# Optimization experiments

Measured on AMD Instinct MI355X. Metric: run time of the kernel, lower is better.

The kernel has to match this reference:

```python
import jax, jax.numpy as jnp
import numpy as np

NUM_HEADS = 4
HEAD_DIM = 64
BN_EPS = 1e-5


def setup_inputs() -> dict:
    key = jax.random.key(0)
    ks = jax.random.split(key, 6)
    B, C, H, W = 8, 256, 48, 48
    HD = NUM_HEADS * HEAD_DIM  # 256
    x = jax.random.normal(ks[0], (B, C, H, W), dtype=jnp.float32)
    q_w = jax.random.normal(ks[1], (HD, C), dtype=jnp.float32) * (1.0 / np.sqrt(C))
    k_w = jax.random.normal(ks[2], (HEAD_DIM, C), dtype=jnp.float32) * (1.0 / np.sqrt(C))
    v_w = jax.random.normal(ks[3], (HEAD_DIM, C), dtype=jnp.float32) * (1.0 / np.sqrt(C))
    proj_w = jax.random.normal(ks[4], (C, HD), dtype=jnp.float32) * (1.0 / np.sqrt(HD))
    proj_b = jnp.zeros((C,), dtype=jnp.float32)
    gamma = jnp.ones((C,), dtype=jnp.float32)
    beta = jnp.zeros((C,), dtype=jnp.float32)
    return {"x": x, "q_w": q_w, "k_w": k_w, "v_w": v_w,
            "proj_w": proj_w, "proj_b": proj_b, "gamma": gamma, "beta": beta}


def reference(x, q_w, k_w, v_w, proj_w, proj_b, gamma, beta):
    B, C, H, W = x.shape
    N = H * W
    scale = HEAD_DIM ** -0.5
    xf = x.reshape(B, C, N)  # 1x1 conv == channel matmul
    q = jnp.einsum('oc,bcn->bon', q_w, xf).reshape(B, NUM_HEADS, HEAD_DIM, N)
    k = jnp.einsum('dc,bcn->bdn', k_w, xf)  # shared single KV head (MQA)
    v = jnp.einsum('dc,bcn->bdn', v_w, xf)
    # scores: [B, heads, N, N]
    attn = jnp.einsum('bhdn,bdm->bhnm', q, k) * scale
    attn = jax.nn.softmax(attn, axis=-1)
    out = jnp.einsum('bhnm,bdm->bhdn', attn, v)  # [B, heads, d, N]
    out = out.reshape(B, NUM_HEADS * HEAD_DIM, N)
    out = jnp.einsum('co,bon->bcn', proj_w, out) + proj_b[None, :, None]
    out = out.reshape(B, C, H, W)
    # BatchNorm2d (training-mode batch statistics, biased variance)
    mean = jnp.mean(out, axis=(0, 2, 3), keepdims=True)
    var = jnp.var(out, axis=(0, 2, 3), keepdims=True)
    out = gamma[None, :, None, None] * (out - mean) * jax.lax.rsqrt(var + BN_EPS) + beta[None, :, None, None]
    return out + x
```

## Files before the change

### kernel.cpp

```cpp
#include <hip/hip_runtime.h>
#include <hip/hip_bf16.h>
#include <math.h>

#define BB 8
#define CCH 256
#define NN 2304
#define NH 4
#define HDIM 64
#define QKV_ROWS 384
#define BN_EPS 1e-5f
#define NTILES 36
#define SLOG2E 0.18033688011112042f

typedef short bf16x8 __attribute__((ext_vector_type(8)));
typedef float f32x4 __attribute__((ext_vector_type(4)));

#if __has_builtin(__builtin_amdgcn_exp2f)
#define EXP2(x) __builtin_amdgcn_exp2f(x)
#else
#define EXP2(x) __expf((x) * 0.6931471805599453f)
#endif

__device__ __forceinline__ unsigned bfpair(float a, float b) {
    __hip_bfloat162 h = __float22bfloat162_rn(make_float2(a, b));
    return *(unsigned*)&h;
}
__device__ __forceinline__ unsigned short f2bf(float f) {
    unsigned u = __float_as_uint(f);
    u = (u + 0x7FFFu + ((u >> 16) & 1u)) >> 16;
    return (unsigned short)u;
}

__global__ __launch_bounds__(256) void cvt_x_k(
    const float* __restrict__ x, unsigned short* __restrict__ xT)
{
    __shared__ float sX[64][65];
    const int tid = threadIdx.x;
    const int b  = blockIdx.x;
    const int nb = blockIdx.y * 64;
    const int cb = blockIdx.z * 64;

    #pragma unroll
    for (int u = 0; u < 4; ++u) {
        int c  = (tid >> 4) + 16 * u;
        int n4 = (tid & 15) * 4;
        float4 v = *(const float4*)(x + ((size_t)(b * CCH + cb + c)) * NN + nb + n4);
        sX[c][n4+0] = v.x; sX[c][n4+1] = v.y; sX[c][n4+2] = v.z; sX[c][n4+3] = v.w;
    }
    __syncthreads();

    const int n  = tid >> 2;
    const int cg = (tid & 3) * 16;
    unsigned vals[8];
    #pragma unroll
    for (int p = 0; p < 8; ++p)
        vals[p] = bfpair(sX[cg + 2*p][n], sX[cg + 2*p + 1][n]);
    unsigned short* dst = xT + ((size_t)(b * NN + nb + n)) * CCH + cb + cg;
    *(uint4*)dst = make_uint4(vals[0], vals[1], vals[2], vals[3]);
    *(uint4*)(dst + 8) = make_uint4(vals[4], vals[5], vals[6], vals[7]);
}

__global__ __launch_bounds__(256) void cvt_w_k(
    const float* __restrict__ qw, const float* __restrict__ kw,
    const float* __restrict__ vw, const float* __restrict__ pw,
    unsigned short* __restrict__ Wb, unsigned short* __restrict__ Pb)
{
    int idx = blockIdx.x * 256 + threadIdx.x;
    if (idx < 98304) {
        int o = idx >> 8, c = idx & 255;
        float v;
        if (o < 256)      v = qw[(size_t)o * CCH + c] * SLOG2E;
        else if (o < 320) v = kw[(size_t)(o - 256) * CCH + c];
        else              v = vw[(size_t)(o - 320) * CCH + c];
        Wb[idx] = f2bf(v);
    } else {
        int j = idx - 98304;
        if (j < 65536) Pb[j] = f2bf(pw[j]);
    }
}

__global__ __launch_bounds__(128) void qkv_mfma_k(
    const unsigned short* __restrict__ Wb, const unsigned short* __restrict__ xT,
    unsigned short* __restrict__ Qt, unsigned short* __restrict__ Kt,
    unsigned short* __restrict__ Vn)
{
    __shared__ unsigned short sE[2][64 * 72];
    const int tid = threadIdx.x;
    const int wave = tid >> 6;
    const int lane = tid & 63;
    const int quad = lane >> 4;
    const int l15  = lane & 15;
    const int b  = blockIdx.x;
    const int nb = blockIdx.y * 64;
    const int mb = blockIdx.z * 128 + wave * 64;

    const unsigned short* Ab = Wb + (size_t)(mb + l15) * CCH + quad * 8;
    const unsigned short* Bb = xT + ((size_t)(b * NN + nb + l15)) * CCH + quad * 8;

    f32x4 C[4][4] = {};
    for (int k0 = 0; k0 < CCH; k0 += 32) {
        bf16x8 aA[4], bB[4];
        #pragma unroll
        for (int i = 0; i < 4; ++i) aA[i] = *(const bf16x8*)(Ab + (size_t)(16*i) * CCH + k0);
        #pragma unroll
        for (int j = 0; j < 4; ++j) bB[j] = *(const bf16x8*)(Bb + (size_t)(16*j) * CCH + k0);
        #pragma unroll
        for (int i = 0; i < 4; ++i)
            #pragma unroll
            for (int j = 0; j < 4; ++j)
                C[i][j] = __builtin_amdgcn_mfma_f32_16x16x32_bf16(aA[i], bB[j], C[i][j], 0, 0, 0);
    }

    unsigned short* sEw = &sE[wave][0];
    if (mb < 320) {
        #pragma unroll
        for (int i = 0; i < 4; ++i)
            #pragma unroll
            for (int j = 0; j < 4; ++j) {
                unsigned p01 = bfpair(C[i][j][0], C[i][j][1]);
                unsigned p23 = bfpair(C[i][j][2], C[i][j][3]);
                unsigned short* p = sEw + (16*j + l15) * 72 + 16*i + quad*4;
                *(unsigned*)p = p01;
                *(unsigned*)(p + 2) = p23;
            }
        if (mb < 256) {
            #pragma unroll
            for (int it = 0; it < 8; ++it) {
                int flat = lane + 64 * it;
                int row = flat >> 3;
                int o8  = (flat & 7) * 8;
                uint4 v = *(const uint4*)(sEw + row * 72 + o8);
                *(uint4*)(Qt + ((size_t)(b * NN + nb + row)) * CCH + mb + o8) = v;
            }
        } else {
            #pragma unroll
            for (int it = 0; it < 8; ++it) {
                int flat = lane + 64 * it;
                int row = flat >> 3;
                int o8  = (flat & 7) * 8;
                uint4 v = *(const uint4*)(sEw + row * 72 + o8);
                *(uint4*)(Kt + ((size_t)(b * NN + nb + row)) * 64 + o8) = v;
            }
        }
    } else {
        #pragma unroll
        for (int i = 0; i < 4; ++i)
            #pragma unroll
            for (int j = 0; j < 4; ++j) {
                unsigned p01 = bfpair(C[i][j][0], C[i][j][1]);
                unsigned p23 = bfpair(C[i][j][2], C[i][j][3]);
                unsigned short* p = sEw + (16*i + quad*4) * 72 + 16*j + l15;
                p[0]   = (unsigned short)p01;
                p[72]  = (unsigned short)(p01 >> 16);
                p[144] = (unsigned short)p23;
                p[216] = (unsigned short)(p23 >> 16);
            }
        #pragma unroll
        for (int it = 0; it < 8; ++it) {
            int flat = lane + 64 * it;
            int row = flat >> 3;
            int n8  = (flat & 7) * 8;
            uint4 v = *(const uint4*)(sEw + row * 72 + n8);
            *(uint4*)(Vn + ((size_t)(b * 64 + (mb - 320) + row)) * NN + nb + n8) = v;
        }
    }
}

__global__ __launch_bounds__(256) void attn_k(
    const unsigned short* __restrict__ Qt,
    const unsigned short* __restrict__ Kt,
    const unsigned short* __restrict__ Vn,
    unsigned short* __restrict__ Ao)
{
    __shared__ __align__(16) char smem[36864];
    unsigned short* sK = (unsigned short*)smem;
    unsigned short* sV = (unsigned short*)(smem + 9216);
    unsigned short* sP = (unsigned short*)(smem + 18432);
    unsigned short* sT = (unsigned short*)smem;

    const int tid  = threadIdx.x;
    const int wave = tid >> 6;
    const int lane = tid & 63;
    const int quad = lane >> 4;
    const int l15  = lane & 15;
    const int hloc = wave >> 1;
    const int qoff = (wave & 1) * 32;
    const int b    = blockIdx.x;
    const int nb   = blockIdx.y * 64;
    const int head = blockIdx.z * 2 + hloc;

    unsigned short* sPh = sP + hloc * 64 * 72;

    bf16x8 aQ[2][2];
    const unsigned short* QtB = Qt + ((size_t)(b * NN + nb + qoff + l15)) * CCH + head * 64 + quad * 8;
    #pragma unroll
    for (int i = 0; i < 2; ++i)
        #pragma unroll
        for (int s = 0; s < 2; ++s)
            aQ[i][s] = *(const bf16x8*)(QtB + (size_t)(16*i) * CCH + s * 32);

    const int srow = tid >> 3;
    const int sch  = (tid & 7) * 8;

    bf16x8 pK[2], pV[2];
    #pragma unroll
    for (int u = 0; u < 2; ++u) {
        int row = srow + 32 * u;
        pK[u] = *(const bf16x8*)(Kt + ((size_t)(b * NN + row)) * 64 + sch);
        pV[u] = *(const bf16x8*)(Vn + ((size_t)(b * 64 + row)) * NN + sch);
    }

    f32x4 O[2][4] = {};
    float lacc[2][4] = {};

    for (int t = 0; t < NTILES; ++t) {
        __syncthreads();
        #pragma unroll
        for (int u = 0; u < 2; ++u) {
            int row = srow + 32 * u;
            *(bf16x8*)(sK + row * 72 + sch) = pK[u];
            *(bf16x8*)(sV + row * 72 + sch) = pV[u];
        }
        __syncthreads();

        if (t + 1 < NTILES) {
            const int m0n = (t + 1) * 64;
            #pragma unroll
            for (int u = 0; u < 2; ++u) {
                int row = srow + 32 * u;
                pK[u] = *(const bf16x8*)(Kt + ((size_t)(b * NN + m0n + row)) * 64 + sch);
                pV[u] = *(const bf16x8*)(Vn + ((size_t)(b * 64 + row)) * NN + m0n + sch);
            }
        }

        f32x4 C[2][4] = {};
        #pragma unroll
        for (int s = 0; s < 2; ++s)
            #pragma unroll
            for (int j = 0; j < 4; ++j) {
                bf16x8 bK = *(const bf16x8*)(sK + (16*j + l15) * 72 + s * 32 + quad * 8);
                C[0][j] = __builtin_amdgcn_mfma_f32_16x16x32_bf16(aQ[0][s], bK, C[0][j], 0, 0, 0);
                C[1][j] = __builtin_amdgcn_mfma_f32_16x16x32_bf16(aQ[1][s], bK, C[1][j], 0, 0, 0);
            }

        #pragma unroll
        for (int i = 0; i < 2; ++i)
            #pragma unroll
            for (int j = 0; j < 4; ++j) {
                float p0 = EXP2(C[i][j][0]);
                float p1 = EXP2(C[i][j][1]);
                float p2 = EXP2(C[i][j][2]);
                float p3 = EXP2(C[i][j][3]);
                lacc[i][0] += p0; lacc[i][1] += p1; lacc[i][2] += p2; lacc[i][3] += p3;
                unsigned p01 = bfpair(p0, p1);
                unsigned p23 = bfpair(p2, p3);
                unsigned short* bp = sPh + (qoff + 16*i + quad*4) * 72 + 16*j + l15;
                bp[0]   = (unsigned short)p01;
                bp[72]  = (unsigned short)(p01 >> 16);
                bp[144] = (unsigned short)p23;
                bp[216] = (unsigned short)(p23 >> 16);
            }

        #pragma unroll
        for (int s = 0; s < 2; ++s) {
            bf16x8 aP0 = *(const bf16x8*)(sPh + (qoff +  0 + l15) * 72 + s * 32 + quad * 8);
            bf16x8 aP1 = *(const bf16x8*)(sPh + (qoff + 16 + l15) * 72 + s * 32 + quad * 8);
            #pragma unroll
            for (int jd = 0; jd < 4; ++jd) {
                bf16x8 bV = *(const bf16x8*)(sV + (16*jd + l15) * 72 + s * 32 + quad * 8);
                O[0][jd] = __builtin_amdgcn_mfma_f32_16x16x32_bf16(aP0, bV, O[0][jd], 0, 0, 0);
                O[1][jd] = __builtin_amdgcn_mfma_f32_16x16x32_bf16(aP1, bV, O[1][jd], 0, 0, 0);
            }
        }
    }

    float rinv[2][4];
    #pragma unroll
    for (int i = 0; i < 2; ++i)
        #pragma unroll
        for (int r = 0; r < 4; ++r) {
            float s = lacc[i][r];
            s += __shfl_xor(s, 1);
            s += __shfl_xor(s, 2);
            s += __shfl_xor(s, 4);
            s += __shfl_xor(s, 8);
            rinv[i][r] = 1.0f / s;
        }

    __syncthreads();
    #pragma unroll
    for (int i = 0; i < 2; ++i)
        #pragma unroll
        for (int jd = 0; jd < 4; ++jd)
            #pragma unroll
            for (int r = 0; r < 4; ++r)
                sT[(qoff + 16*i + quad*4 + r) * 136 + hloc * 64 + 16*jd + l15] =
                    f2bf(O[i][jd][r] * rinv[i][r]);
    __syncthreads();

    #pragma unroll
    for (int it = 0; it < 4; ++it) {
        int flat = tid + 256 * it;
        int row = flat >> 4;
        int c8  = (flat & 15) * 8;
        uint4 v = *(const uint4*)(sT + row * 136 + c8);
        *(uint4*)(Ao + ((size_t)(b * NN + nb + row)) * CCH + blockIdx.z * 128 + c8) = v;
    }
}

__global__ __launch_bounds__(128) void proj_mfma_k(
    const unsigned short* __restrict__ Pb, const unsigned short* __restrict__ Ao,
    const float* __restrict__ pb, float* __restrict__ proj)
{
    __shared__ float sF[2][64 * 68];
    const int tid = threadIdx.x;
    const int wave = tid >> 6;
    const int lane = tid & 63;
    const int quad = lane >> 4;
    const int l15  = lane & 15;
    const int b  = blockIdx.x;
    const int nb = blockIdx.y * 64;
    const int mb = blockIdx.z * 128 + wave * 64;

    const unsigned short* Ab = Pb + (size_t)(mb + l15) * CCH + quad * 8;
    const unsigned short* Bb = Ao + ((size_t)(b * NN + nb + l15)) * CCH + quad * 8;

    f32x4 C[4][4] = {};
    for (int k0 = 0; k0 < CCH; k0 += 32) {
        bf16x8 aA[4], bB[4];
        #pragma unroll
        for (int i = 0; i < 4; ++i) aA[i] = *(const bf16x8*)(Ab + (size_t)(16*i) * CCH + k0);
        #pragma unroll
        for (int j = 0; j < 4; ++j) bB[j] = *(const bf16x8*)(Bb + (size_t)(16*j) * CCH + k0);
        #pragma unroll
        for (int i = 0; i < 4; ++i)
            #pragma unroll
            for (int j = 0; j < 4; ++j)
                C[i][j] = __builtin_amdgcn_mfma_f32_16x16x32_bf16(aA[i], bB[j], C[i][j], 0, 0, 0);
    }

    float* sFw = &sF[wave][0];
    #pragma unroll
    for (int i = 0; i < 4; ++i)
        #pragma unroll
        for (int r = 0; r < 4; ++r) {
            float bias = pb[mb + 16*i + quad*4 + r];
            #pragma unroll
            for (int j = 0; j < 4; ++j)
                sFw[(16*i + quad*4 + r) * 68 + 16*j + l15] = C[i][j][r] + bias;
        }
    #pragma unroll
    for (int it = 0; it < 16; ++it) {
        int flat = lane + 64 * it;
        int row = flat >> 4;
        int ch  = (flat & 15) * 4;
        f32x4 v = *(const f32x4*)(sFw + row * 68 + ch);
        *(f32x4*)(proj + ((size_t)(b * CCH + mb + row)) * NN + nb + ch) = v;
    }
}

__global__ __launch_bounds__(256) void bn_stats_k(
    const float* __restrict__ proj, const float* __restrict__ gamma,
    const float* __restrict__ beta, float* __restrict__ stats)
{
    const int c = blockIdx.x;
    const int tid = threadIdx.x;
    float s = 0.f, s2 = 0.f;
    for (int b = 0; b < BB; ++b) {
        const float* p = proj + ((size_t)b * CCH + c) * NN;
        for (int n = tid * 4; n < NN; n += 1024) {
            float4 v = *(const float4*)(p + n);
            s  += v.x + v.y + v.z + v.w;
            s2 += v.x*v.x + v.y*v.y + v.z*v.z + v.w*v.w;
        }
    }
    __shared__ float rs[256], rs2[256];
    rs[tid] = s; rs2[tid] = s2;
    __syncthreads();
    for (int off = 128; off > 0; off >>= 1) {
        if (tid < off) { rs[tid] += rs[tid + off]; rs2[tid] += rs2[tid + off]; }
        __syncthreads();
    }
    if (tid == 0) {
        const float inv_n = 1.0f / (float)(BB * NN);
        float mean = rs[0] * inv_n;
        float var  = rs2[0] * inv_n - mean * mean;
        float sc = gamma[c] * rsqrtf(var + BN_EPS);
        stats[c] = sc;
        stats[CCH + c] = beta[c] - mean * sc;
    }
}

__global__ __launch_bounds__(256) void bn_apply_k(
    const float* __restrict__ proj, const float* __restrict__ x,
    const float* __restrict__ stats, float* __restrict__ out)
{
    size_t idx = ((size_t)blockIdx.x * 256 + threadIdx.x) * 4;
    const size_t total = (size_t)BB * CCH * NN;
    if (idx >= total) return;
    int c = (int)((idx / NN) % CCH);
    float sc = stats[c], sh = stats[CCH + c];
    float4 p  = *(const float4*)(proj + idx);
    float4 xv = *(const float4*)(x + idx);
    float4 r;
    r.x = sc * p.x + sh + xv.x;
    r.y = sc * p.y + sh + xv.y;
    r.z = sc * p.z + sh + xv.z;
    r.w = sc * p.w + sh + xv.w;
    *(float4*)(out + idx) = r;
}

extern "C" void kernel_launch(void* const* d_in, const int* in_sizes, int n_in,
                              void* d_out, int out_size, void* d_ws, size_t ws_size,
                              hipStream_t stream)
{
    const float* x     = (const float*)d_in[0];
    const float* qw    = (const float*)d_in[1];
    const float* kw    = (const float*)d_in[2];
    const float* vw    = (const float*)d_in[3];
    const float* pw    = (const float*)d_in[4];
    const float* pb    = (const float*)d_in[5];
    const float* gamma = (const float*)d_in[6];
    const float* beta  = (const float*)d_in[7];
    float* out = (float*)d_out;

    char* ws = (char*)d_ws;
    unsigned short* xT = (unsigned short*)ws;
    unsigned short* Ao = (unsigned short*)ws;
    unsigned short* Wb = (unsigned short*)(ws + 9437184);
    unsigned short* Pb = (unsigned short*)(ws + 9633792);
    unsigned short* Qt = (unsigned short*)(ws + 9764864);
    unsigned short* Kt = (unsigned short*)(ws + 19202048);
    unsigned short* Vn = (unsigned short*)(ws + 21561344);
    float* proj  = (float*)(ws + 9764864);
    float* stats = (float*)(ws + 28639232);

    cvt_w_k<<<640, 256, 0, stream>>>(qw, kw, vw, pw, Wb, Pb);

    dim3 g0(BB, NN / 64, CCH / 64);
    cvt_x_k<<<g0, 256, 0, stream>>>(x, xT);

    dim3 g1(BB, NN / 64, 3);
    qkv_mfma_k<<<g1, 128, 0, stream>>>(Wb, xT, Qt, Kt, Vn);

    dim3 g2(BB, NN / 64, NH / 2);
    attn_k<<<g2, 256, 0, stream>>>(Qt, Kt, Vn, Ao);

    dim3 g3(BB, NN / 64, 2);
    proj_mfma_k<<<g3, 128, 0, stream>>>(Pb, Ao, pb, proj);

    bn_stats_k<<<CCH, 256, 0, stream>>>(proj, gamma, beta, stats);

    int total4 = BB * CCH * NN / 4;
    bn_apply_k<<<(total4 + 255) / 256, 256, 0, stream>>>(proj, x, stats, out);
}
```

Baseline: 224.6 us.

## Keep attention probabilities in registers, fuse BN stats into projection, store bf16

The attention kernel is restructured to one head per 128-thread block. It computes transposed scores (K times Q) so the exponentiated probabilities feed the PV MFMA directly from registers as 16x16x16 operands, removing the LDS round trip for P. The projection kernel now adds bias, reduces per-channel sum and sum of squares via shuffles and atomics, and stores the output as bf16. This replaces the separate BN statistics pass and halves the intermediate traffic. The risks are extra rounding from bf16 storage and from single-pass variance, plus atomic contention.

```diff
diff --git a/kernel.cpp b/kernel.cpp
--- a/kernel.cpp
+++ b/kernel.cpp
@@ -13,6 +13,7 @@
 #define SLOG2E 0.18033688011112042f
 
 typedef short bf16x8 __attribute__((ext_vector_type(8)));
+typedef short bf16x4 __attribute__((ext_vector_type(4)));
 typedef float f32x4 __attribute__((ext_vector_type(4)));
 
 #if __has_builtin(__builtin_amdgcn_exp2f)
@@ -21,6 +22,9 @@
 #define EXP2(x) __expf((x) * 0.6931471805599453f)
 #endif
 
+#define MFMA16(a, b, c) __builtin_amdgcn_mfma_f32_16x16x16bf16_1k(a, b, c, 0, 0, 0)
+#define MFMA32(a, b, c) __builtin_amdgcn_mfma_f32_16x16x32_bf16(a, b, c, 0, 0, 0)
+
 __device__ __forceinline__ unsigned bfpair(float a, float b) {
     __hip_bfloat162 h = __float22bfloat162_rn(make_float2(a, b));
     return *(unsigned*)&h;
@@ -29,6 +33,15 @@
     unsigned u = __float_as_uint(f);
     u = (u + 0x7FFFu + ((u >> 16) & 1u)) >> 16;
     return (unsigned short)u;
+}
+__device__ __forceinline__ bf16x4 pack4(float p0, float p1, float p2, float p3) {
+    union { unsigned u[2]; bf16x4 v; } x;
+    x.u[0] = bfpair(p0, p1);
+    x.u[1] = bfpair(p2, p3);
+    return x.v;
+}
+__device__ __forceinline__ float bf2f(unsigned short s) {
+    return __uint_as_float((unsigned)s << 16);
 }
 
 __global__ __launch_bounds__(256) void cvt_x_k(
@@ -63,7 +76,8 @@
 __global__ __launch_bounds__(256) void cvt_w_k(
     const float* __restrict__ qw, const float* __restrict__ kw,
     const float* __restrict__ vw, const float* __restrict__ pw,
-    unsigned short* __restrict__ Wb, unsigned short* __restrict__ Pb)
+    unsigned short* __restrict__ Wb, unsigned short* __restrict__ Pb,
+    float* __restrict__ ssum, float* __restrict__ ssq)
 {
     int idx = blockIdx.x * 256 + threadIdx.x;
     if (idx < 98304) {
@@ -76,6 +90,11 @@
     } else {
         int j = idx - 98304;
         if (j < 65536) Pb[j] = f2bf(pw[j]);
+        else {
+            int z = j - 65536;
+            if (z < 256)      ssum[z] = 0.f;
+            else if (z < 512) ssq[z - 256] = 0.f;
+        }
     }
 }
 
@@ -108,7 +127,7 @@
         for (int i = 0; i < 4; ++i)
             #pragma unroll
             for (int j = 0; j < 4; ++j)
-                C[i][j] = __builtin_amdgcn_mfma_f32_16x16x32_bf16(aA[i], bB[j], C[i][j], 0, 0, 0);
+                C[i][j] = MFMA32(aA[i], bB[j], C[i][j]);
     }
 
     unsigned short* sEw = &sE[wave][0];
@@ -166,153 +185,142 @@
     }
 }
 
-__global__ __launch_bounds__(256) void attn_k(
+__global__ __launch_bounds__(128) void attn_k(
     const unsigned short* __restrict__ Qt,
     const unsigned short* __restrict__ Kt,
     const unsigned short* __restrict__ Vn,
     unsigned short* __restrict__ Ao)
 {
-    __shared__ __align__(16) char smem[36864];
-    unsigned short* sK = (unsigned short*)smem;
-    unsigned short* sV = (unsigned short*)(smem + 9216);
-    unsigned short* sP = (unsigned short*)(smem + 18432);
-    unsigned short* sT = (unsigned short*)smem;
+    __shared__ __align__(16) unsigned short sKV[2 * 64 * 72];
+    unsigned short* sK = sKV;
+    unsigned short* sV = sKV + 64 * 72;
+    unsigned short* sT = sKV;
 
     const int tid  = threadIdx.x;
     const int wave = tid >> 6;
     const int lane = tid & 63;
     const int quad = lane >> 4;
     const int l15  = lane & 15;
-    const int hloc = wave >> 1;
-    const int qoff = (wave & 1) * 32;
     const int b    = blockIdx.x;
     const int nb   = blockIdx.y * 64;
-    const int head = blockIdx.z * 2 + hloc;
-
-    unsigned short* sPh = sP + hloc * 64 * 72;
-
-    bf16x8 aQ[2][2];
+    const int head = blockIdx.z;
+    const int qoff = wave * 32;
+
+    bf16x8 bQ[2][2];
     const unsigned short* QtB = Qt + ((size_t)(b * NN + nb + qoff + l15)) * CCH + head * 64 + quad * 8;
     #pragma unroll
-    for (int i = 0; i < 2; ++i)
+    for (int qt = 0; qt < 2; ++qt)
         #pragma unroll
         for (int s = 0; s < 2; ++s)
-            aQ[i][s] = *(const bf16x8*)(QtB + (size_t)(16*i) * CCH + s * 32);
-
-    const int srow = tid >> 3;
-    const int sch  = (tid & 7) * 8;
-
-    bf16x8 pK[2], pV[2];
-    #pragma unroll
-    for (int u = 0; u < 2; ++u) {
-        int row = srow + 32 * u;
-        pK[u] = *(const bf16x8*)(Kt + ((size_t)(b * NN + row)) * 64 + sch);
-        pV[u] = *(const bf16x8*)(Vn + ((size_t)(b * 64 + row)) * NN + sch);
-    }
-
-    f32x4 O[2][4] = {};
-    float lacc[2][4] = {};
+            bQ[qt][s] = *(const bf16x8*)(QtB + (size_t)(16*qt) * CCH + s * 32);
+
+    bf16x8 pK[4], pV[4];
+    #pragma unroll
+    for (int u = 0; u < 4; ++u) {
+        int flat = tid + 128 * u;
+        int row = flat >> 3;
+        int ch  = (flat & 7) * 8;
+        pK[u] = *(const bf16x8*)(Kt + ((size_t)(b * NN + row)) * 64 + ch);
+        pV[u] = *(const bf16x8*)(Vn + ((size_t)(b * 64 + row)) * NN + ch);
+    }
+
+    f32x4 O[4][2] = {};
+    float lacc[2] = {0.f, 0.f};
 
     for (int t = 0; t < NTILES; ++t) {
         __syncthreads();
         #pragma unroll
-        for (int u = 0; u < 2; ++u) {
-            int row = srow + 32 * u;
-            *(bf16x8*)(sK + row * 72 + sch) = pK[u];
-            *(bf16x8*)(sV + row * 72 + sch) = pV[u];
+        for (int u = 0; u < 4; ++u) {
+            int flat = tid + 128 * u;
+            int row = flat >> 3;
+            int ch  = (flat & 7) * 8;
+            *(bf16x8*)(sK + row * 72 + ch) = pK[u];
+            *(bf16x8*)(sV + row * 72 + ch) = pV[u];
         }
         __syncthreads();
 
         if (t + 1 < NTILES) {
             const int m0n = (t + 1) * 64;
             #pragma unroll
-            for (int u = 0; u < 2; ++u) {
-                int row = srow + 32 * u;
-                pK[u] = *(const bf16x8*)(Kt + ((size_t)(b * NN + m0n + row)) * 64 + sch);
-                pV[u] = *(const bf16x8*)(Vn + ((size_t)(b * 64 + row)) * NN + m0n + sch);
-            }
-        }
-
-        f32x4 C[2][4] = {};
+            for (int u = 0; u < 4; ++u) {
+                int flat = tid + 128 * u;
+                int row = flat >> 3;
+                int ch  = (flat & 7) * 8;
+                pK[u] = *(const bf16x8*)(Kt + ((size_t)(b * NN + m0n + row)) * 64 + ch);
+                pV[u] = *(const bf16x8*)(Vn + ((size_t)(b * 64 + row)) * NN + m0n + ch);
+            }
+        }
+
+        f32x4 C[4][2] = {};
         #pragma unroll
         for (int s = 0; s < 2; ++s)
             #pragma unroll
-            for (int j = 0; j < 4; ++j) {
-                bf16x8 bK = *(const bf16x8*)(sK + (16*j + l15) * 72 + s * 32 + quad * 8);
-                C[0][j] = __builtin_amdgcn_mfma_f32_16x16x32_bf16(aQ[0][s], bK, C[0][j], 0, 0, 0);
-                C[1][j] = __builtin_amdgcn_mfma_f32_16x16x32_bf16(aQ[1][s], bK, C[1][j], 0, 0, 0);
-            }
-
-        #pragma unroll
-        for (int i = 0; i < 2; ++i)
-            #pragma unroll
-            for (int j = 0; j < 4; ++j) {
-                float p0 = EXP2(C[i][j][0]);
-                float p1 = EXP2(C[i][j][1]);
-                float p2 = EXP2(C[i][j][2]);
-                float p3 = EXP2(C[i][j][3]);
-                lacc[i][0] += p0; lacc[i][1] += p1; lacc[i][2] += p2; lacc[i][3] += p3;
-                unsigned p01 = bfpair(p0, p1);
-                unsigned p23 = bfpair(p2, p3);
-                unsigned short* bp = sPh + (qoff + 16*i + quad*4) * 72 + 16*j + l15;
-                bp[0]   = (unsigned short)p01;
-                bp[72]  = (unsigned short)(p01 >> 16);
-                bp[144] = (unsigned short)p23;
-                bp[216] = (unsigned short)(p23 >> 16);
-            }
-
-        #pragma unroll
-        for (int s = 0; s < 2; ++s) {
-            bf16x8 aP0 = *(const bf16x8*)(sPh + (qoff +  0 + l15) * 72 + s * 32 + quad * 8);
-            bf16x8 aP1 = *(const bf16x8*)(sPh + (qoff + 16 + l15) * 72 + s * 32 + quad * 8);
-            #pragma unroll
-            for (int jd = 0; jd < 4; ++jd) {
-                bf16x8 bV = *(const bf16x8*)(sV + (16*jd + l15) * 72 + s * 32 + quad * 8);
-                O[0][jd] = __builtin_amdgcn_mfma_f32_16x16x32_bf16(aP0, bV, O[0][jd], 0, 0, 0);
-                O[1][jd] = __builtin_amdgcn_mfma_f32_16x16x32_bf16(aP1, bV, O[1][jd], 0, 0, 0);
-            }
-        }
-    }
-
-    float rinv[2][4];
-    #pragma unroll
-    for (int i = 0; i < 2; ++i)
-        #pragma unroll
-        for (int r = 0; r < 4; ++r) {
-            float s = lacc[i][r];
-            s += __shfl_xor(s, 1);
-            s += __shfl_xor(s, 2);
-            s += __shfl_xor(s, 4);
-            s += __shfl_xor(s, 8);
-            rinv[i][r] = 1.0f / s;
-        }
+            for (int kt = 0; kt < 4; ++kt) {
+                bf16x8 aK = *(const bf16x8*)(sK + (16*kt + l15) * 72 + s * 32 + quad * 8);
+                C[kt][0] = MFMA32(aK, bQ[0][s], C[kt][0]);
+                C[kt][1] = MFMA32(aK, bQ[1][s], C[kt][1]);
+            }
+
+        bf16x4 bP[4][2];
+        #pragma unroll
+        for (int kt = 0; kt < 4; ++kt)
+            #pragma unroll
+            for (int qt = 0; qt < 2; ++qt) {
+                float p0 = EXP2(C[kt][qt][0]);
+                float p1 = EXP2(C[kt][qt][1]);
+                float p2 = EXP2(C[kt][qt][2]);
+                float p3 = EXP2(C[kt][qt][3]);
+                lacc[qt] += (p0 + p1) + (p2 + p3);
+                bP[kt][qt] = pack4(p0, p1, p2, p3);
+            }
+
+        #pragma unroll
+        for (int jd = 0; jd < 4; ++jd)
+            #pragma unroll
+            for (int kt = 0; kt < 4; ++kt) {
+                bf16x4 aV = *(const bf16x4*)(sV + (16*jd + l15) * 72 + 16*kt + quad*4);
+                O[jd][0] = MFMA16(aV, bP[kt][0], O[jd][0]);
+                O[jd][1] = MFMA16(aV, bP[kt][1], O[jd][1]);
+            }
+    }
+
+    float rinv[2];
+    #pragma unroll
+    for (int qt = 0; qt < 2; ++qt) {
+        float s = lacc[qt];
+        s += __shfl_xor(s, 16);
+        s += __shfl_xor(s, 32);
+        rinv[qt] = 1.0f / s;
+    }
 
     __syncthreads();
     #pragma unroll
-    for (int i = 0; i < 2; ++i)
-        #pragma unroll
-        for (int jd = 0; jd < 4; ++jd)
-            #pragma unroll
-            for (int r = 0; r < 4; ++r)
-                sT[(qoff + 16*i + quad*4 + r) * 136 + hloc * 64 + 16*jd + l15] =
-                    f2bf(O[i][jd][r] * rinv[i][r]);
+    for (int qt = 0; qt < 2; ++qt)
+        #pragma unroll
+        for (int jd = 0; jd < 4; ++jd) {
+            unsigned lo = bfpair(O[jd][qt][0] * rinv[qt], O[jd][qt][1] * rinv[qt]);
+            unsigned hi = bfpair(O[jd][qt][2] * rinv[qt], O[jd][qt][3] * rinv[qt]);
+            uint2 w = make_uint2(lo, hi);
+            *(uint2*)(sT + (qoff + 16*qt + l15) * 72 + 16*jd + quad*4) = w;
+        }
     __syncthreads();
 
     #pragma unroll
     for (int it = 0; it < 4; ++it) {
-        int flat = tid + 256 * it;
-        int row = flat >> 4;
-        int c8  = (flat & 15) * 8;
-        uint4 v = *(const uint4*)(sT + row * 136 + c8);
-        *(uint4*)(Ao + ((size_t)(b * NN + nb + row)) * CCH + blockIdx.z * 128 + c8) = v;
+        int flat = tid + 128 * it;
+        int row = flat >> 3;
+        int c8  = (flat & 7) * 8;
+        uint4 v = *(const uint4*)(sT + row * 72 + c8);
+        *(uint4*)(Ao + ((size_t)(b * NN + nb + row)) * CCH + head * 64 + c8) = v;
     }
 }
 
 __global__ __launch_bounds__(128) void proj_mfma_k(
     const unsigned short* __restrict__ Pb, const unsigned short* __restrict__ Ao,
-    const float* __restrict__ pb, float* __restrict__ proj)
-{
-    __shared__ float sF[2][64 * 68];
+    const float* __restrict__ pb, unsigned short* __restrict__ projb,
+    float* __restrict__ ssum, float* __restrict__ ssq)
+{
+    __shared__ unsigned short sE[2][64 * 72];
     const int tid = threadIdx.x;
     const int wave = tid >> 6;
     const int lane = tid & 63;
@@ -336,78 +344,92 @@
         for (int i = 0; i < 4; ++i)
             #pragma unroll
             for (int j = 0; j < 4; ++j)
-                C[i][j] = __builtin_amdgcn_mfma_f32_16x16x32_bf16(aA[i], bB[j], C[i][j], 0, 0, 0);
-    }
-
-    float* sFw = &sF[wave][0];
+                C[i][j] = MFMA32(aA[i], bB[j], C[i][j]);
+    }
+
+    unsigned short* sEw = &sE[wave][0];
+    #pragma unroll
+    for (int i = 0; i < 4; ++i) {
+        #pragma unroll
+        for (int r = 0; r < 4; ++r) {
+            const int ch = mb + 16*i + quad*4 + r;
+            const float bias = pb[ch];
+            float v0 = C[i][0][r] + bias, v1 = C[i][1][r] + bias;
+            float v2 = C[i][2][r] + bias, v3 = C[i][3][r] + bias;
+            C[i][0][r] = v0; C[i][1][r] = v1; C[i][2][r] = v2; C[i][3][r] = v3;
+            float rs = (v0 + v1) + (v2 + v3);
+            float rq = (v0*v0 + v1*v1) + (v2*v2 + v3*v3);
+            rs += __shfl_xor(rs, 1); rq += __shfl_xor(rq, 1);
+            rs += __shfl_xor(rs, 2); rq += __shfl_xor(rq, 2);
+            rs += __shfl_xor(rs, 4); rq += __shfl_xor(rq, 4);
+            rs += __shfl_xor(rs, 8); rq += __shfl_xor(rq, 8);
+            if (l15 == 0) {
+                atomicAdd(&ssum[ch], rs);
+                atomicAdd(&ssq[ch], rq);
+            }
+        }
+    }
+
     #pragma unroll
     for (int i = 0; i < 4; ++i)
         #pragma unroll
-        for (int r = 0; r < 4; ++r) {
-            float bias = pb[mb + 16*i + quad*4 + r];
-            #pragma unroll
-            for (int j = 0; j < 4; ++j)
-                sFw[(16*i + quad*4 + r) * 68 + 16*j + l15] = C[i][j][r] + bias;
-        }
-    #pragma unroll
-    for (int it = 0; it < 16; ++it) {
+        for (int j = 0; j < 4; ++j) {
+            unsigned p01 = bfpair(C[i][j][0], C[i][j][1]);
+            unsigned p23 = bfpair(C[i][j][2], C[i][j][3]);
+            unsigned short* p = sEw + (16*i + quad*4) * 72 + 16*j + l15;
+            p[0]   = (unsigned short)p01;
+            p[72]  = (unsigned short)(p01 >> 16);
+            p[144] = (unsigned short)p23;
+            p[216] = (unsigned short)(p23 >> 16);
+        }
+    #pragma unroll
+    for (int it = 0; it < 8; ++it) {
         int flat = lane + 64 * it;
-        int row = flat >> 4;
-        int ch  = (flat & 15) * 4;
-        f32x4 v = *(const f32x4*)(sFw + row * 68 + ch);
-        *(f32x4*)(proj + ((size_t)(b * CCH + mb + row)) * NN + nb + ch) = v;
-    }
-}
-
-__global__ __launch_bounds__(256) void bn_stats_k(
-    const float* __restrict__ proj, const float* __restrict__ gamma,
-    const float* __restrict__ beta, float* __restrict__ stats)
-{
-    const int c = blockIdx.x;
-    const int tid = threadIdx.x;
-    float s = 0.f, s2 = 0.f;
-    for (int b = 0; b < BB; ++b) {
-        const float* p = proj + ((size_t)b * CCH + c) * NN;
-        for (int n = tid * 4; n < NN; n += 1024) {
-            float4 v = *(const float4*)(p + n);
-            s  += v.x + v.y + v.z + v.w;
-            s2 += v.x*v.x + v.y*v.y + v.z*v.z + v.w*v.w;
-        }
-    }
-    __shared__ float rs[256], rs2[256];
-    rs[tid] = s; rs2[tid] = s2;
-    __syncthreads();
-    for (int off = 128; off > 0; off >>= 1) {
-        if (tid < off) { rs[tid] += rs[tid + off]; rs2[tid] += rs2[tid + off]; }
-        __syncthreads();
-    }
-    if (tid == 0) {
-        const float inv_n = 1.0f / (float)(BB * NN);
-        float mean = rs[0] * inv_n;
-        float var  = rs2[0] * inv_n - mean * mean;
-        float sc = gamma[c] * rsqrtf(var + BN_EPS);
-        stats[c] = sc;
-        stats[CCH + c] = beta[c] - mean * sc;
-    }
+        int row = flat >> 3;
+        int n8  = (flat & 7) * 8;
+        uint4 v = *(const uint4*)(sEw + row * 72 + n8);
+        *(uint4*)(projb + ((size_t)(b * CCH + mb + row)) * NN + nb + n8) = v;
+    }
+}
+
+__global__ __launch_bounds__(256) void bn_finalize_k(
+    const float* __restrict__ ssum, const float* __restrict__ ssq,
+    const float* __restrict__ gamma, const float* __restrict__ beta,
+    float* __restrict__ stats)
+{
+    const int c = threadIdx.x;
+    const float inv_n = 1.0f / (float)(BB * NN);
+    float mean = ssum[c] * inv_n;
+    float var  = ssq[c] * inv_n - mean * mean;
+    float sc = gamma[c] * rsqrtf(var + BN_EPS);
+    stats[c] = sc;
+    stats[CCH + c] = beta[c] - mean * sc;
 }
 
 __global__ __launch_bounds__(256) void bn_apply_k(
-    const float* __restrict__ proj, const float* __restrict__ x,
+    const unsigned short* __restrict__ projb, const float* __restrict__ x,
     const float* __restrict__ stats, float* __restrict__ out)
 {
-    size_t idx = ((size_t)blockIdx.x * 256 + threadIdx.x) * 4;
+    size_t idx = ((size_t)blockIdx.x * 256 + threadIdx.x) * 8;
     const size_t total = (size_t)BB * CCH * NN;
     if (idx >= total) return;
     int c = (int)((idx / NN) % CCH);
     float sc = stats[c], sh = stats[CCH + c];
-    float4 p  = *(const float4*)(proj + idx);
-    float4 xv = *(const float4*)(x + idx);
-    float4 r;
-    r.x = sc * p.x + sh + xv.x;
-    r.y = sc * p.y + sh + xv.y;
-    r.z = sc * p.z + sh + xv.z;
-    r.w = sc * p.w + sh + xv.w;
-    *(float4*)(out + idx) = r;
+    uint4 pv = *(const uint4*)(projb + idx);
+    const unsigned short* ps = (const unsigned short*)&pv;
+    float4 x0 = *(const float4*)(x + idx);
+    float4 x1 = *(const float4*)(x + idx + 4);
+    float4 r0, r1;
+    r0.x = sc * bf2f(ps[0]) + sh + x0.x;
+    r0.y = sc * bf2f(ps[1]) + sh + x0.y;
+    r0.z = sc * bf2f(ps[2]) + sh + x0.z;
+    r0.w = sc * bf2f(ps[3]) + sh + x0.w;
+    r1.x = sc * bf2f(ps[4]) + sh + x1.x;
+    r1.y = sc * bf2f(ps[5]) + sh + x1.y;
+    r1.z = sc * bf2f(ps[6]) + sh + x1.z;
+    r1.w = sc * bf2f(ps[7]) + sh + x1.w;
+    *(float4*)(out + idx) = r0;
+    *(float4*)(out + idx + 4) = r1;
 }
 
 extern "C" void kernel_launch(void* const* d_in, const int* in_sizes, int n_in,
@@ -432,10 +454,12 @@
     unsigned short* Qt = (unsigned short*)(ws + 9764864);
     unsigned short* Kt = (unsigned short*)(ws + 19202048);
     unsigned short* Vn = (unsigned short*)(ws + 21561344);
-    float* proj  = (float*)(ws + 9764864);
+    unsigned short* projb = (unsigned short*)(ws + 9764864);
     float* stats = (float*)(ws + 28639232);
-
-    cvt_w_k<<<640, 256, 0, stream>>>(qw, kw, vw, pw, Wb, Pb);
+    float* ssum  = (float*)(ws + 28641280);
+    float* ssq   = (float*)(ws + 28642304);
+
+    cvt_w_k<<<642, 256, 0, stream>>>(qw, kw, vw, pw, Wb, Pb, ssum, ssq);
 
     dim3 g0(BB, NN / 64, CCH / 64);
     cvt_x_k<<<g0, 256, 0, stream>>>(x, xT);
@@ -443,14 +467,14 @@
     dim3 g1(BB, NN / 64, 3);
     qkv_mfma_k<<<g1, 128, 0, stream>>>(Wb, xT, Qt, Kt, Vn);
 
-    dim3 g2(BB, NN / 64, NH / 2);
-    attn_k<<<g2, 256, 0, stream>>>(Qt, Kt, Vn, Ao);
+    dim3 g2(BB, NN / 64, NH);
+    attn_k<<<g2, 128, 0, stream>>>(Qt, Kt, Vn, Ao);
 
     dim3 g3(BB, NN / 64, 2);
-    proj_mfma_k<<<g3, 128, 0, stream>>>(Pb, Ao, pb, proj);
-
-    bn_stats_k<<<CCH, 256, 0, stream>>>(proj, gamma, beta, stats);
-
-    int total4 = BB * CCH * NN / 4;
-    bn_apply_k<<<(total4 + 255) / 256, 256, 0, stream>>>(proj, x, stats, out);
-}
+    proj_mfma_k<<<g3, 128, 0, stream>>>(Pb, Ao, pb, projb, ssum, ssq);
+
+    bn_finalize_k<<<1, 256, 0, stream>>>(ssum, ssq, gamma, beta, stats);
+
+    int total8 = BB * CCH * NN / 8;
+    bn_apply_k<<<(total8 + 255) / 256, 256, 0, stream>>>(projb, x, stats, out);
+}
```

Measured after the change: 244.0 us. 8.7% more time.
